# Kernel optimization log

Measured on AMD Instinct MI355X. Metric: run time of the kernel, lower is better.

## Reference

```python
import jax, jax.numpy as jnp
import numpy as np

M, D, I, E, TOPK = 2048, 1024, 2048, 8, 2

def setup_inputs() -> dict:
    key = jax.random.key(0)
    k1, k2, k3, k4 = jax.random.split(key, 4)
    x = jax.random.normal(k1, (M, D), dtype=jnp.float32)
    w13 = jax.random.normal(k2, (E, 2 * I, D), dtype=jnp.float32) * 0.02
    w2 = jax.random.normal(k3, (E, D, I), dtype=jnp.float32) * 0.02
    expert_indices = jax.random.randint(k4, (M, TOPK), 0, E, dtype=jnp.int64)
    return {"x": x, "w13": w13, "w2": w2, "expert_indices": expert_indices}

def reference(x, w13, w2, expert_indices):
    # Faithful to the 'gpt-fast' math: per (token, slot) SiLU-gated expert FFN.
    # Instead of gathering per-token weight copies (huge), compute each expert's
    # FFN densely over all tokens, then gather the selected expert output.
    inter = w2.shape[2]

    def per_expert(w13_e, w2_e):
        h = jnp.einsum('md,nd->mn', x, w13_e)          # [M, 2I]
        x1, x3 = h[:, :inter], h[:, inter:]
        return jnp.einsum('mi,di->md', jax.nn.silu(x1) * x3, w2_e)  # [M, D]

    outs = jax.vmap(per_expert)(w13, w2)               # [E, M, D]
    outs = jnp.transpose(outs, (1, 0, 2))              # [M, E, D]
    # out[t, a] = outs[t, expert_indices[t, a]]
    idx = expert_indices[..., None]                    # [M, TOPK, 1]
    return jnp.take_along_axis(outs, idx, axis=1)      # [M, TOPK, D]
```

## Files before the change

kernel.cpp:

```cpp
#include <hip/hip_runtime.h>
#include <hip/hip_bf16.h>
#include <cstdint>
#include <cstddef>

#define DDIM  1024
#define IDIM  2048
#define NEXP  8
#define NPAIR 4096
#define MAXTILE 40

typedef __attribute__((ext_vector_type(8))) short short8;
typedef __attribute__((ext_vector_type(4))) float floatx4;
typedef __attribute__((ext_vector_type(4))) float fvec4;

__device__ inline short8 pack8v(fvec4 a, fvec4 b) {
    union { short8 s8; __hip_bfloat162 h[4]; } u;
    u.h[0] = __float22bfloat162_rn(float2{a.x, a.y});
    u.h[1] = __float22bfloat162_rn(float2{a.z, a.w});
    u.h[2] = __float22bfloat162_rn(float2{b.x, b.y});
    u.h[3] = __float22bfloat162_rn(float2{b.z, b.w});
    return u.s8;
}

__device__ inline void gload_lds16(const unsigned short* g, unsigned short* l) {
    __builtin_amdgcn_global_load_lds((const __attribute__((address_space(1))) void*)g,
                                     (__attribute__((address_space(3))) void*)l, 16, 0, 0);
}

__launch_bounds__(256)
__global__ void cvt_all(const fvec4* __restrict__ x, const fvec4* __restrict__ w13,
                        const fvec4* __restrict__ w2,
                        uint4* __restrict__ xb, uint4* __restrict__ w13b,
                        uint4* __restrict__ w2b) {
    const int t = threadIdx.x;
    for (int job = blockIdx.x; job < 6400; job += gridDim.x) {
        const fvec4* src; uint4* dst; int cbase;
        if (job < 4096)      { src = w13; dst = w13b; cbase = job << 10; }
        else if (job < 6144) { src = w2;  dst = w2b;  cbase = (job - 4096) << 10; }
        else                 { src = x;   dst = xb;   cbase = (job - 6144) << 10; }
        const int c0 = cbase + t;
        fvec4 a0 = __builtin_nontemporal_load(src + 2 * (c0 + 0));
        fvec4 b0 = __builtin_nontemporal_load(src + 2 * (c0 + 0) + 1);
        fvec4 a1 = __builtin_nontemporal_load(src + 2 * (c0 + 256));
        fvec4 b1 = __builtin_nontemporal_load(src + 2 * (c0 + 256) + 1);
        fvec4 a2 = __builtin_nontemporal_load(src + 2 * (c0 + 512));
        fvec4 b2 = __builtin_nontemporal_load(src + 2 * (c0 + 512) + 1);
        fvec4 a3 = __builtin_nontemporal_load(src + 2 * (c0 + 768));
        fvec4 b3 = __builtin_nontemporal_load(src + 2 * (c0 + 768) + 1);
        __builtin_amdgcn_sched_barrier(0);
        short8 p0 = pack8v(a0, b0);
        short8 p1 = pack8v(a1, b1);
        short8 p2 = pack8v(a2, b2);
        short8 p3 = pack8v(a3, b3);
        dst[c0 + 0]   = *(uint4*)&p0;
        dst[c0 + 256] = *(uint4*)&p1;
        dst[c0 + 512] = *(uint4*)&p2;
        dst[c0 + 768] = *(uint4*)&p3;
    }
}

__global__ void route_kernel(const int* __restrict__ eidx,
                             int4* __restrict__ tbl,
                             int* __restrict__ slot_q) {
    __shared__ int cnt[NEXP];
    __shared__ int cur[NEXP];
    const int t = threadIdx.x;
    if (t < NEXP) cnt[t] = 0;
    __syncthreads();
    for (int q = t; q < NPAIR; q += 1024) atomicAdd(&cnt[eidx[q]], 1);
    __syncthreads();
    if (t == 0) {
        int s = 0, nt = 0;
        for (int e = 0; e < NEXP; e++) {
            cur[e] = s;
            for (int mb = 0; mb < cnt[e]; mb += 128)
                tbl[nt++] = int4{e, mb, s, cnt[e]};
            s += cnt[e];
        }
        for (; nt < MAXTILE; nt++) tbl[nt] = int4{0, 0, 0, 0};
    }
    __syncthreads();
    for (int q = t; q < NPAIR; q += 1024) {
        int e = eidx[q];
        int pos = atomicAdd(&cur[e], 1);
        slot_q[pos] = q;
    }
}

__launch_bounds__(256)
__global__ void gemm1_swiglu(const unsigned short* __restrict__ xb,
                             const unsigned short* __restrict__ w13b,
                             const int4* __restrict__ tbl,
                             const int* __restrict__ slot_q,
                             unsigned short* __restrict__ pbuf) {
    const int4 tt = tbl[blockIdx.y];
    const int e = tt.x, mbase = tt.y, off0 = tt.z, ne = tt.w;
    if (mbase >= ne) return;
    const int n0 = blockIdx.x * 64;

    __shared__ __align__(16) unsigned short As[128 * 64];
    __shared__ __align__(16) unsigned short Bs[128 * 64];

    const int t    = threadIdx.x;
    const int lane = t & 63;
    const int wid  = t >> 6;

    const int rr = t >> 3;
    const int g  = (t & 7) ^ (rr & 7);
    const unsigned short* pA[4];
    const unsigned short* pB[4];
    const unsigned short* wb1 = w13b + (size_t)e * (2 * IDIM) * DDIM;
    #pragma unroll
    for (int c = 0; c < 4; c++) {
        int row = c * 32 + rr;
        int sl = mbase + row; if (sl > ne - 1) sl = ne - 1;
        pA[c] = xb + (size_t)(slot_q[off0 + sl] >> 1) * DDIM + g * 8;
        int wrow = (row < 64) ? (n0 + row) : (IDIM + n0 + (row - 64));
        pB[c] = wb1 + (size_t)wrow * DDIM + g * 8;
    }
    unsigned short* lA = As + wid * 512;
    unsigned short* lB = Bs + wid * 512;

    const int wm = wid >> 1, wn = wid & 1;
    const int quad = lane >> 4, l16 = lane & 15;
    const int rsw = l16 & 7;
    const int co0 = (quad ^ rsw) * 8;
    const int co1 = ((quad + 4) ^ rsw) * 8;

    floatx4 acc1[4][2], acc3[4][2];
    #pragma unroll
    for (int i = 0; i < 4; i++)
        #pragma unroll
        for (int j = 0; j < 2; j++) {
            acc1[i][j] = floatx4{0.f, 0.f, 0.f, 0.f};
            acc3[i][j] = floatx4{0.f, 0.f, 0.f, 0.f};
        }

    for (int it = 0; it < DDIM / 64; ++it) {
        const int ko = it * 64;
        __syncthreads();
        #pragma unroll
        for (int c = 0; c < 4; c++) {
            gload_lds16(pA[c] + ko, lA + c * 2048);
            gload_lds16(pB[c] + ko, lB + c * 2048);
        }
        __syncthreads();

        #pragma unroll
        for (int h = 0; h < 2; ++h) {
            const int co = h ? co1 : co0;
            short8 af[4], b1f[2], b3f[2];
            #pragma unroll
            for (int mi = 0; mi < 4; mi++)
                af[mi] = *(short8*)&As[(wm * 64 + mi * 16 + l16) * 64 + co];
            #pragma unroll
            for (int ni = 0; ni < 2; ni++) {
                b1f[ni] = *(short8*)&Bs[(wn * 32 + ni * 16 + l16) * 64 + co];
                b3f[ni] = *(short8*)&Bs[(64 + wn * 32 + ni * 16 + l16) * 64 + co];
            }
            #pragma unroll
            for (int mi = 0; mi < 4; mi++)
                #pragma unroll
                for (int ni = 0; ni < 2; ni++) {
                    acc1[mi][ni] = __builtin_amdgcn_mfma_f32_16x16x32_bf16(af[mi], b1f[ni], acc1[mi][ni], 0, 0, 0);
                    acc3[mi][ni] = __builtin_amdgcn_mfma_f32_16x16x32_bf16(af[mi], b3f[ni], acc3[mi][ni], 0, 0, 0);
                }
        }
    }

    #pragma unroll
    for (int mi = 0; mi < 4; mi++) {
        #pragma unroll
        for (int ni = 0; ni < 2; ni++) {
            const int col = n0 + wn * 32 + ni * 16 + l16;
            #pragma unroll
            for (int rw = 0; rw < 4; rw++) {
                const int s2 = mbase + wm * 64 + mi * 16 + quad * 4 + rw;
                if (s2 < ne) {
                    float v1 = acc1[mi][ni][rw];
                    float v3 = acc3[mi][ni][rw];
                    float pv = v1 / (1.f + __expf(-v1)) * v3;
                    __hip_bfloat16 pb = __float2bfloat16(pv);
                    pbuf[(size_t)(off0 + s2) * IDIM + col] = *(unsigned short*)&pb;
                }
            }
        }
    }
}

__launch_bounds__(256)
__global__ void gemm2_out(const unsigned short* __restrict__ pbuf,
                          const unsigned short* __restrict__ w2b,
                          const int4* __restrict__ tbl,
                          const int* __restrict__ slot_q,
                          float* __restrict__ out) {
    const int4 tt = tbl[blockIdx.y];
    const int e = tt.x, mbase = tt.y, off0 = tt.z, ne = tt.w;
    if (mbase >= ne) return;
    const int n0 = blockIdx.x * 64;

    __shared__ __align__(16) unsigned short As[128 * 64];
    __shared__ __align__(16) unsigned short Bs[64 * 64];

    const int t    = threadIdx.x;
    const int lane = t & 63;
    const int wid  = t >> 6;

    const int rr = t >> 3;
    const int g  = (t & 7) ^ (rr & 7);
    const unsigned short* pA[4];
    const unsigned short* pB[2];
    const unsigned short* wb = w2b + (size_t)e * DDIM * IDIM;
    #pragma unroll
    for (int c = 0; c < 4; c++) {
        int row = c * 32 + rr;
        int sl = mbase + row; if (sl > ne - 1) sl = ne - 1;
        pA[c] = pbuf + (size_t)(off0 + sl) * IDIM + g * 8;
    }
    #pragma unroll
    for (int c = 0; c < 2; c++) {
        int row = c * 32 + rr;
        pB[c] = wb + (size_t)(n0 + row) * IDIM + g * 8;
    }
    unsigned short* lA = As + wid * 512;
    unsigned short* lB = Bs + wid * 512;

    const int wm = wid >> 1, wn = wid & 1;
    const int quad = lane >> 4, l16 = lane & 15;
    const int rsw = l16 & 7;
    const int co0 = (quad ^ rsw) * 8;
    const int co1 = ((quad + 4) ^ rsw) * 8;

    floatx4 acc[4][2];
    #pragma unroll
    for (int i = 0; i < 4; i++)
        #pragma unroll
        for (int j = 0; j < 2; j++) acc[i][j] = floatx4{0.f, 0.f, 0.f, 0.f};

    for (int it = 0; it < IDIM / 64; ++it) {
        const int ko = it * 64;
        __syncthreads();
        #pragma unroll
        for (int c = 0; c < 4; c++)
            gload_lds16(pA[c] + ko, lA + c * 2048);
        #pragma unroll
        for (int c = 0; c < 2; c++)
            gload_lds16(pB[c] + ko, lB + c * 2048);
        __syncthreads();

        #pragma unroll
        for (int h = 0; h < 2; ++h) {
            const int co = h ? co1 : co0;
            short8 af[4], bf[2];
            #pragma unroll
            for (int mi = 0; mi < 4; mi++)
                af[mi] = *(short8*)&As[(wm * 64 + mi * 16 + l16) * 64 + co];
            #pragma unroll
            for (int ni = 0; ni < 2; ni++)
                bf[ni] = *(short8*)&Bs[(wn * 32 + ni * 16 + l16) * 64 + co];
            #pragma unroll
            for (int mi = 0; mi < 4; mi++)
                #pragma unroll
                for (int ni = 0; ni < 2; ni++)
                    acc[mi][ni] = __builtin_amdgcn_mfma_f32_16x16x32_bf16(af[mi], bf[ni], acc[mi][ni], 0, 0, 0);
        }
    }

    #pragma unroll
    for (int mi = 0; mi < 4; mi++) {
        #pragma unroll
        for (int rw = 0; rw < 4; rw++) {
            const int s2 = mbase + wm * 64 + mi * 16 + quad * 4 + rw;
            if (s2 < ne) {
                const int qq = slot_q[off0 + s2];
                float* orow = out + (size_t)qq * DDIM;
                #pragma unroll
                for (int ni = 0; ni < 2; ni++)
                    orow[n0 + wn * 32 + ni * 16 + l16] = acc[mi][ni][rw];
            }
        }
    }
}

extern "C" void kernel_launch(void* const* d_in, const int* in_sizes, int n_in,
                              void* d_out, int out_size, void* d_ws, size_t ws_size,
                              hipStream_t stream) {
    const float* x    = (const float*)d_in[0];
    const float* w13  = (const float*)d_in[1];
    const float* w2   = (const float*)d_in[2];
    const int*   eidx = (const int*)d_in[3];
    float* out = (float*)d_out;

    const size_t OFF_XB   = 65536;
    const size_t OFF_W13B = OFF_XB + (size_t)4 * 1024 * 1024;
    const size_t OFF_W2B  = OFF_W13B + (size_t)64 * 1024 * 1024;
    const size_t OFF_PBUF = OFF_W2B + (size_t)32 * 1024 * 1024;

    int4* tbl   = (int4*)((char*)d_ws + 128);
    int* slot_q = (int*)((char*)d_ws + 1024);
    unsigned short* xb   = (unsigned short*)((char*)d_ws + OFF_XB);
    unsigned short* w13b = (unsigned short*)((char*)d_ws + OFF_W13B);
    unsigned short* w2b  = (unsigned short*)((char*)d_ws + OFF_W2B);
    unsigned short* pbuf = (unsigned short*)((char*)d_ws + OFF_PBUF);

    hipLaunchKernelGGL(route_kernel, dim3(1), dim3(1024), 0, stream, eidx, tbl, slot_q);
    hipLaunchKernelGGL(cvt_all, dim3(6400), dim3(256), 0, stream,
                       (const fvec4*)x, (const fvec4*)w13, (const fvec4*)w2,
                       (uint4*)xb, (uint4*)w13b, (uint4*)w2b);
    hipLaunchKernelGGL(gemm1_swiglu, dim3(IDIM / 64, MAXTILE), dim3(256), 0, stream,
                       xb, w13b, tbl, slot_q, pbuf);
    hipLaunchKernelGGL(gemm2_out, dim3(DDIM / 64, MAXTILE), dim3(256), 0, stream,
                       pbuf, w2b, tbl, slot_q, out);
}
```

Measured before the change: 342.7 us.

## Enlarge GEMM tiles and add XCD-aware block swizzle for grouped MoE GEMMs

gemm1 moves to 256x128 tiles (512 threads, separate 256-row routing table) and gemm2 widens its N tile to 128, so each block reuses its loaded A and B data across more MFMA work and fewer blocks re-read the same rows. Both GEMMs also remap block IDs so that neighbouring tiles land on the same XCD, aiming for better L2 locality. The cost is more LDS and accumulator registers per block, which may lower occupancy, plus fewer blocks in the grid, which may leave CUs idle.

```diff
diff --git a/kernel.cpp b/kernel.cpp
--- a/kernel.cpp
+++ b/kernel.cpp
@@ -7,7 +7,8 @@
 #define IDIM  2048
 #define NEXP  8
 #define NPAIR 4096
-#define MAXTILE 40
+#define MAXT1 24
+#define MAXT2 40
 
 typedef __attribute__((ext_vector_type(8))) short short8;
 typedef __attribute__((ext_vector_type(4))) float floatx4;
@@ -25,6 +26,13 @@
 __device__ inline void gload_lds16(const unsigned short* g, unsigned short* l) {
     __builtin_amdgcn_global_load_lds((const __attribute__((address_space(1))) void*)g,
                                      (__attribute__((address_space(3))) void*)l, 16, 0, 0);
+}
+
+__device__ inline void xcd_swz(int gridX, int nwg, int& bx, int& by) {
+    const int lin = by * gridX + bx;
+    const int q = nwg >> 3;
+    const int swz = (lin & 7) * q + (lin >> 3);
+    bx = swz % gridX; by = swz / gridX;
 }
 
 __launch_bounds__(256)
@@ -60,7 +68,8 @@
 }
 
 __global__ void route_kernel(const int* __restrict__ eidx,
-                             int4* __restrict__ tbl,
+                             int4* __restrict__ tbl1,
+                             int4* __restrict__ tbl2,
                              int* __restrict__ slot_q) {
     __shared__ int cnt[NEXP];
     __shared__ int cur[NEXP];
@@ -70,14 +79,17 @@
     for (int q = t; q < NPAIR; q += 1024) atomicAdd(&cnt[eidx[q]], 1);
     __syncthreads();
     if (t == 0) {
-        int s = 0, nt = 0;
+        int s = 0, n1 = 0, n2 = 0;
         for (int e = 0; e < NEXP; e++) {
             cur[e] = s;
+            for (int mb = 0; mb < cnt[e]; mb += 256)
+                tbl1[n1++] = int4{e, mb, s, cnt[e]};
             for (int mb = 0; mb < cnt[e]; mb += 128)
-                tbl[nt++] = int4{e, mb, s, cnt[e]};
+                tbl2[n2++] = int4{e, mb, s, cnt[e]};
             s += cnt[e];
         }
-        for (; nt < MAXTILE; nt++) tbl[nt] = int4{0, 0, 0, 0};
+        for (; n1 < MAXT1; n1++) tbl1[n1] = int4{0, 0, 0, 0};
+        for (; n2 < MAXT2; n2++) tbl2[n2] = int4{0, 0, 0, 0};
     }
     __syncthreads();
     for (int q = t; q < NPAIR; q += 1024) {
@@ -87,19 +99,21 @@
     }
 }
 
-__launch_bounds__(256)
+__launch_bounds__(512)
 __global__ void gemm1_swiglu(const unsigned short* __restrict__ xb,
                              const unsigned short* __restrict__ w13b,
                              const int4* __restrict__ tbl,
                              const int* __restrict__ slot_q,
                              unsigned short* __restrict__ pbuf) {
-    const int4 tt = tbl[blockIdx.y];
+    int bx = blockIdx.x, by = blockIdx.y;
+    xcd_swz(16, 16 * MAXT1, bx, by);
+    const int4 tt = tbl[by];
     const int e = tt.x, mbase = tt.y, off0 = tt.z, ne = tt.w;
     if (mbase >= ne) return;
-    const int n0 = blockIdx.x * 64;
-
-    __shared__ __align__(16) unsigned short As[128 * 64];
-    __shared__ __align__(16) unsigned short Bs[128 * 64];
+    const int n0 = bx * 128;
+
+    __shared__ __align__(16) unsigned short As[256 * 64];
+    __shared__ __align__(16) unsigned short Bs[256 * 64];
 
     const int t    = threadIdx.x;
     const int lane = t & 63;
@@ -112,24 +126,24 @@
     const unsigned short* wb1 = w13b + (size_t)e * (2 * IDIM) * DDIM;
     #pragma unroll
     for (int c = 0; c < 4; c++) {
-        int row = c * 32 + rr;
+        int row = c * 64 + rr;
         int sl = mbase + row; if (sl > ne - 1) sl = ne - 1;
         pA[c] = xb + (size_t)(slot_q[off0 + sl] >> 1) * DDIM + g * 8;
-        int wrow = (row < 64) ? (n0 + row) : (IDIM + n0 + (row - 64));
+        int wrow = (row < 128) ? (n0 + row) : (IDIM + n0 + (row - 128));
         pB[c] = wb1 + (size_t)wrow * DDIM + g * 8;
     }
     unsigned short* lA = As + wid * 512;
     unsigned short* lB = Bs + wid * 512;
 
-    const int wm = wid >> 1, wn = wid & 1;
+    const int wm = wid >> 2, wn = wid & 3;
     const int quad = lane >> 4, l16 = lane & 15;
     const int rsw = l16 & 7;
     const int co0 = (quad ^ rsw) * 8;
     const int co1 = ((quad + 4) ^ rsw) * 8;
 
-    floatx4 acc1[4][2], acc3[4][2];
-    #pragma unroll
-    for (int i = 0; i < 4; i++)
+    floatx4 acc1[8][2], acc3[8][2];
+    #pragma unroll
+    for (int i = 0; i < 8; i++)
         #pragma unroll
         for (int j = 0; j < 2; j++) {
             acc1[i][j] = floatx4{0.f, 0.f, 0.f, 0.f};
@@ -141,25 +155,25 @@
         __syncthreads();
         #pragma unroll
         for (int c = 0; c < 4; c++) {
-            gload_lds16(pA[c] + ko, lA + c * 2048);
-            gload_lds16(pB[c] + ko, lB + c * 2048);
+            gload_lds16(pA[c] + ko, lA + c * 4096);
+            gload_lds16(pB[c] + ko, lB + c * 4096);
         }
         __syncthreads();
 
         #pragma unroll
         for (int h = 0; h < 2; ++h) {
             const int co = h ? co1 : co0;
-            short8 af[4], b1f[2], b3f[2];
-            #pragma unroll
-            for (int mi = 0; mi < 4; mi++)
-                af[mi] = *(short8*)&As[(wm * 64 + mi * 16 + l16) * 64 + co];
+            short8 af[8], b1f[2], b3f[2];
+            #pragma unroll
+            for (int mi = 0; mi < 8; mi++)
+                af[mi] = *(short8*)&As[(wm * 128 + mi * 16 + l16) * 64 + co];
             #pragma unroll
             for (int ni = 0; ni < 2; ni++) {
                 b1f[ni] = *(short8*)&Bs[(wn * 32 + ni * 16 + l16) * 64 + co];
-                b3f[ni] = *(short8*)&Bs[(64 + wn * 32 + ni * 16 + l16) * 64 + co];
+                b3f[ni] = *(short8*)&Bs[(128 + wn * 32 + ni * 16 + l16) * 64 + co];
             }
             #pragma unroll
-            for (int mi = 0; mi < 4; mi++)
+            for (int mi = 0; mi < 8; mi++)
                 #pragma unroll
                 for (int ni = 0; ni < 2; ni++) {
                     acc1[mi][ni] = __builtin_amdgcn_mfma_f32_16x16x32_bf16(af[mi], b1f[ni], acc1[mi][ni], 0, 0, 0);
@@ -169,13 +183,13 @@
     }
 
     #pragma unroll
-    for (int mi = 0; mi < 4; mi++) {
+    for (int mi = 0; mi < 8; mi++) {
         #pragma unroll
         for (int ni = 0; ni < 2; ni++) {
             const int col = n0 + wn * 32 + ni * 16 + l16;
             #pragma unroll
             for (int rw = 0; rw < 4; rw++) {
-                const int s2 = mbase + wm * 64 + mi * 16 + quad * 4 + rw;
+                const int s2 = mbase + wm * 128 + mi * 16 + quad * 4 + rw;
                 if (s2 < ne) {
                     float v1 = acc1[mi][ni][rw];
                     float v3 = acc3[mi][ni][rw];
@@ -194,13 +208,15 @@
                           const int4* __restrict__ tbl,
                           const int* __restrict__ slot_q,
                           float* __restrict__ out) {
-    const int4 tt = tbl[blockIdx.y];
+    int bx = blockIdx.x, by = blockIdx.y;
+    xcd_swz(8, 8 * MAXT2, bx, by);
+    const int4 tt = tbl[by];
     const int e = tt.x, mbase = tt.y, off0 = tt.z, ne = tt.w;
     if (mbase >= ne) return;
-    const int n0 = blockIdx.x * 64;
+    const int n0 = bx * 128;
 
     __shared__ __align__(16) unsigned short As[128 * 64];
-    __shared__ __align__(16) unsigned short Bs[64 * 64];
+    __shared__ __align__(16) unsigned short Bs[128 * 64];
 
     const int t    = threadIdx.x;
     const int lane = t & 63;
@@ -209,17 +225,13 @@
     const int rr = t >> 3;
     const int g  = (t & 7) ^ (rr & 7);
     const unsigned short* pA[4];
-    const unsigned short* pB[2];
+    const unsigned short* pB[4];
     const unsigned short* wb = w2b + (size_t)e * DDIM * IDIM;
     #pragma unroll
     for (int c = 0; c < 4; c++) {
         int row = c * 32 + rr;
         int sl = mbase + row; if (sl > ne - 1) sl = ne - 1;
         pA[c] = pbuf + (size_t)(off0 + sl) * IDIM + g * 8;
-    }
-    #pragma unroll
-    for (int c = 0; c < 2; c++) {
-        int row = c * 32 + rr;
         pB[c] = wb + (size_t)(n0 + row) * IDIM + g * 8;
     }
     unsigned short* lA = As + wid * 512;
@@ -231,37 +243,36 @@
     const int co0 = (quad ^ rsw) * 8;
     const int co1 = ((quad + 4) ^ rsw) * 8;
 
-    floatx4 acc[4][2];
+    floatx4 acc[4][4];
     #pragma unroll
     for (int i = 0; i < 4; i++)
         #pragma unroll
-        for (int j = 0; j < 2; j++) acc[i][j] = floatx4{0.f, 0.f, 0.f, 0.f};
+        for (int j = 0; j < 4; j++) acc[i][j] = floatx4{0.f, 0.f, 0.f, 0.f};
 
     for (int it = 0; it < IDIM / 64; ++it) {
         const int ko = it * 64;
         __syncthreads();
         #pragma unroll
-        for (int c = 0; c < 4; c++)
+        for (int c = 0; c < 4; c++) {
             gload_lds16(pA[c] + ko, lA + c * 2048);
-        #pragma unroll
-        for (int c = 0; c < 2; c++)
             gload_lds16(pB[c] + ko, lB + c * 2048);
+        }
         __syncthreads();
 
         #pragma unroll
         for (int h = 0; h < 2; ++h) {
             const int co = h ? co1 : co0;
-            short8 af[4], bf[2];
+            short8 af[4], bf[4];
             #pragma unroll
             for (int mi = 0; mi < 4; mi++)
                 af[mi] = *(short8*)&As[(wm * 64 + mi * 16 + l16) * 64 + co];
             #pragma unroll
-            for (int ni = 0; ni < 2; ni++)
-                bf[ni] = *(short8*)&Bs[(wn * 32 + ni * 16 + l16) * 64 + co];
+            for (int ni = 0; ni < 4; ni++)
+                bf[ni] = *(short8*)&Bs[(wn * 64 + ni * 16 + l16) * 64 + co];
             #pragma unroll
             for (int mi = 0; mi < 4; mi++)
                 #pragma unroll
-                for (int ni = 0; ni < 2; ni++)
+                for (int ni = 0; ni < 4; ni++)
                     acc[mi][ni] = __builtin_amdgcn_mfma_f32_16x16x32_bf16(af[mi], bf[ni], acc[mi][ni], 0, 0, 0);
         }
     }
@@ -275,8 +286,8 @@
                 const int qq = slot_q[off0 + s2];
                 float* orow = out + (size_t)qq * DDIM;
                 #pragma unroll
-                for (int ni = 0; ni < 2; ni++)
-                    orow[n0 + wn * 32 + ni * 16 + l16] = acc[mi][ni][rw];
+                for (int ni = 0; ni < 4; ni++)
+                    orow[n0 + wn * 64 + ni * 16 + l16] = acc[mi][ni][rw];
             }
         }
     }
@@ -296,19 +307,20 @@
     const size_t OFF_W2B  = OFF_W13B + (size_t)64 * 1024 * 1024;
     const size_t OFF_PBUF = OFF_W2B + (size_t)32 * 1024 * 1024;
 
-    int4* tbl   = (int4*)((char*)d_ws + 128);
-    int* slot_q = (int*)((char*)d_ws + 1024);
+    int4* tbl1  = (int4*)((char*)d_ws + 128);
+    int4* tbl2  = (int4*)((char*)d_ws + 2048);
+    int* slot_q = (int*)((char*)d_ws + 4096);
     unsigned short* xb   = (unsigned short*)((char*)d_ws + OFF_XB);
     unsigned short* w13b = (unsigned short*)((char*)d_ws + OFF_W13B);
     unsigned short* w2b  = (unsigned short*)((char*)d_ws + OFF_W2B);
     unsigned short* pbuf = (unsigned short*)((char*)d_ws + OFF_PBUF);
 
-    hipLaunchKernelGGL(route_kernel, dim3(1), dim3(1024), 0, stream, eidx, tbl, slot_q);
+    hipLaunchKernelGGL(route_kernel, dim3(1), dim3(1024), 0, stream, eidx, tbl1, tbl2, slot_q);
     hipLaunchKernelGGL(cvt_all, dim3(6400), dim3(256), 0, stream,
                        (const fvec4*)x, (const fvec4*)w13, (const fvec4*)w2,
                        (uint4*)xb, (uint4*)w13b, (uint4*)w2b);
-    hipLaunchKernelGGL(gemm1_swiglu, dim3(IDIM / 64, MAXTILE), dim3(256), 0, stream,
-                       xb, w13b, tbl, slot_q, pbuf);
-    hipLaunchKernelGGL(gemm2_out, dim3(DDIM / 64, MAXTILE), dim3(256), 0, stream,
-                       pbuf, w2b, tbl, slot_q, out);
-}
+    hipLaunchKernelGGL(gemm1_swiglu, dim3(IDIM / 128, MAXT1), dim3(512), 0, stream,
+                       xb, w13b, tbl1, slot_q, pbuf);
+    hipLaunchKernelGGL(gemm2_out, dim3(DDIM / 128, MAXT2), dim3(256), 0, stream,
+                       pbuf, w2b, tbl2, slot_q, out);
+}
```

Result: slower. 366.1 us (+6.8%).

## Double-buffer LDS tiles in both expert GEMMs to overlap loads with MFMA

Applied to the files above, without the earlier changes.

Both GEMM kernels now keep two LDS stages. The next K tile is issued as a direct global-to-LDS load while MFMAs run on the current tile, with one barrier per iteration instead of two. This aims to hide global memory latency behind compute. Compute sections also raise wave priority with s_setprio. In exchange LDS use doubles (64KB for gemm1), which may lower occupancy.

```diff
diff --git a/kernel.cpp b/kernel.cpp
--- a/kernel.cpp
+++ b/kernel.cpp
@@ -98,8 +98,8 @@
     if (mbase >= ne) return;
     const int n0 = blockIdx.x * 64;
 
-    __shared__ __align__(16) unsigned short As[128 * 64];
-    __shared__ __align__(16) unsigned short Bs[128 * 64];
+    __shared__ __align__(16) unsigned short As[2][128 * 64];
+    __shared__ __align__(16) unsigned short Bs[2][128 * 64];
 
     const int t    = threadIdx.x;
     const int lane = t & 63;
@@ -118,8 +118,7 @@
         int wrow = (row < 64) ? (n0 + row) : (IDIM + n0 + (row - 64));
         pB[c] = wb1 + (size_t)wrow * DDIM + g * 8;
     }
-    unsigned short* lA = As + wid * 512;
-    unsigned short* lB = Bs + wid * 512;
+    const int lo = wid * 512;
 
     const int wm = wid >> 1, wn = wid & 1;
     const int quad = lane >> 4, l16 = lane & 15;
@@ -136,27 +135,37 @@
             acc3[i][j] = floatx4{0.f, 0.f, 0.f, 0.f};
         }
 
+    #pragma unroll
+    for (int c = 0; c < 4; c++) {
+        gload_lds16(pA[c], &As[0][lo + c * 2048]);
+        gload_lds16(pB[c], &Bs[0][lo + c * 2048]);
+    }
+    asm volatile("s_waitcnt vmcnt(0)" ::: "memory");
+    __builtin_amdgcn_s_barrier();
+    __builtin_amdgcn_sched_barrier(0);
+
+    int cur = 0;
     for (int it = 0; it < DDIM / 64; ++it) {
-        const int ko = it * 64;
-        __syncthreads();
-        #pragma unroll
-        for (int c = 0; c < 4; c++) {
-            gload_lds16(pA[c] + ko, lA + c * 2048);
-            gload_lds16(pB[c] + ko, lB + c * 2048);
-        }
-        __syncthreads();
-
+        if (it + 1 < DDIM / 64) {
+            const int ko = (it + 1) * 64;
+            #pragma unroll
+            for (int c = 0; c < 4; c++) {
+                gload_lds16(pA[c] + ko, &As[cur ^ 1][lo + c * 2048]);
+                gload_lds16(pB[c] + ko, &Bs[cur ^ 1][lo + c * 2048]);
+            }
+        }
+        __builtin_amdgcn_s_setprio(1);
         #pragma unroll
         for (int h = 0; h < 2; ++h) {
             const int co = h ? co1 : co0;
             short8 af[4], b1f[2], b3f[2];
             #pragma unroll
             for (int mi = 0; mi < 4; mi++)
-                af[mi] = *(short8*)&As[(wm * 64 + mi * 16 + l16) * 64 + co];
+                af[mi] = *(short8*)&As[cur][(wm * 64 + mi * 16 + l16) * 64 + co];
             #pragma unroll
             for (int ni = 0; ni < 2; ni++) {
-                b1f[ni] = *(short8*)&Bs[(wn * 32 + ni * 16 + l16) * 64 + co];
-                b3f[ni] = *(short8*)&Bs[(64 + wn * 32 + ni * 16 + l16) * 64 + co];
+                b1f[ni] = *(short8*)&Bs[cur][(wn * 32 + ni * 16 + l16) * 64 + co];
+                b3f[ni] = *(short8*)&Bs[cur][(64 + wn * 32 + ni * 16 + l16) * 64 + co];
             }
             #pragma unroll
             for (int mi = 0; mi < 4; mi++)
@@ -166,6 +175,11 @@
                     acc3[mi][ni] = __builtin_amdgcn_mfma_f32_16x16x32_bf16(af[mi], b3f[ni], acc3[mi][ni], 0, 0, 0);
                 }
         }
+        __builtin_amdgcn_s_setprio(0);
+        asm volatile("s_waitcnt vmcnt(0)" ::: "memory");
+        __builtin_amdgcn_s_barrier();
+        __builtin_amdgcn_sched_barrier(0);
+        cur ^= 1;
     }
 
     #pragma unroll
@@ -199,8 +213,8 @@
     if (mbase >= ne) return;
     const int n0 = blockIdx.x * 64;
 
-    __shared__ __align__(16) unsigned short As[128 * 64];
-    __shared__ __align__(16) unsigned short Bs[64 * 64];
+    __shared__ __align__(16) unsigned short As[2][128 * 64];
+    __shared__ __align__(16) unsigned short Bs[2][64 * 64];
 
     const int t    = threadIdx.x;
     const int lane = t & 63;
@@ -222,8 +236,7 @@
         int row = c * 32 + rr;
         pB[c] = wb + (size_t)(n0 + row) * IDIM + g * 8;
     }
-    unsigned short* lA = As + wid * 512;
-    unsigned short* lB = Bs + wid * 512;
+    const int lo = wid * 512;
 
     const int wm = wid >> 1, wn = wid & 1;
     const int quad = lane >> 4, l16 = lane & 15;
@@ -237,33 +250,49 @@
         #pragma unroll
         for (int j = 0; j < 2; j++) acc[i][j] = floatx4{0.f, 0.f, 0.f, 0.f};
 
+    #pragma unroll
+    for (int c = 0; c < 4; c++)
+        gload_lds16(pA[c], &As[0][lo + c * 2048]);
+    #pragma unroll
+    for (int c = 0; c < 2; c++)
+        gload_lds16(pB[c], &Bs[0][lo + c * 2048]);
+    asm volatile("s_waitcnt vmcnt(0)" ::: "memory");
+    __builtin_amdgcn_s_barrier();
+    __builtin_amdgcn_sched_barrier(0);
+
+    int cur = 0;
     for (int it = 0; it < IDIM / 64; ++it) {
-        const int ko = it * 64;
-        __syncthreads();
-        #pragma unroll
-        for (int c = 0; c < 4; c++)
-            gload_lds16(pA[c] + ko, lA + c * 2048);
-        #pragma unroll
-        for (int c = 0; c < 2; c++)
-            gload_lds16(pB[c] + ko, lB + c * 2048);
-        __syncthreads();
-
+        if (it + 1 < IDIM / 64) {
+            const int ko = (it + 1) * 64;
+            #pragma unroll
+            for (int c = 0; c < 4; c++)
+                gload_lds16(pA[c] + ko, &As[cur ^ 1][lo + c * 2048]);
+            #pragma unroll
+            for (int c = 0; c < 2; c++)
+                gload_lds16(pB[c] + ko, &Bs[cur ^ 1][lo + c * 2048]);
+        }
+        __builtin_amdgcn_s_setprio(1);
         #pragma unroll
         for (int h = 0; h < 2; ++h) {
             const int co = h ? co1 : co0;
             short8 af[4], bf[2];
             #pragma unroll
             for (int mi = 0; mi < 4; mi++)
-                af[mi] = *(short8*)&As[(wm * 64 + mi * 16 + l16) * 64 + co];
+                af[mi] = *(short8*)&As[cur][(wm * 64 + mi * 16 + l16) * 64 + co];
             #pragma unroll
             for (int ni = 0; ni < 2; ni++)
-                bf[ni] = *(short8*)&Bs[(wn * 32 + ni * 16 + l16) * 64 + co];
+                bf[ni] = *(short8*)&Bs[cur][(wn * 32 + ni * 16 + l16) * 64 + co];
             #pragma unroll
             for (int mi = 0; mi < 4; mi++)
                 #pragma unroll
                 for (int ni = 0; ni < 2; ni++)
                     acc[mi][ni] = __builtin_amdgcn_mfma_f32_16x16x32_bf16(af[mi], bf[ni], acc[mi][ni], 0, 0, 0);
         }
+        __builtin_amdgcn_s_setprio(0);
+        asm volatile("s_waitcnt vmcnt(0)" ::: "memory");
+        __builtin_amdgcn_s_barrier();
+        __builtin_amdgcn_sched_barrier(0);
+        cur ^= 1;
     }
 
     #pragma unroll
```

Result: no change. 344.0 us (+0.4%).
